# Optimization experiments

Hardware: AMD Instinct MI355X
Metric: run time of the kernel (lower is better)

## Reference

```python
import jax, jax.numpy as jnp
import numpy as np

B, S, D, H, TM = 4, 512, 512, 8, 20
DH = D // H
LAMBDA_REG = 1e-3


def setup_inputs() -> dict:
    key = jax.random.key(0)
    ks = jax.random.split(key, 12)

    def lin(k, o, i):
        return (jax.random.normal(k, (o, i), jnp.float32) / np.float32(np.sqrt(i)))

    return {
        "x": jax.random.normal(ks[0], (B, S, D), jnp.float32),
        "Wq": lin(ks[1], D, D), "Wk": lin(ks[2], D, D), "Wv": lin(ks[3], D, D),
        "Wo": lin(ks[4], D, D), "bo": jnp.zeros((D,), jnp.float32),
        "gw1": lin(ks[5], 64, D), "gb1": jnp.zeros((64,), jnp.float32),
        "gw2": lin(ks[6], 32, 64), "gb2": jnp.zeros((32,), jnp.float32),
        "gw3": lin(ks[7], 1, 32), "gb3": jnp.zeros((1,), jnp.float32),
        "cw1": lin(ks[8], 32, D), "cb1": jnp.zeros((32,), jnp.float32),
        "cw2": lin(ks[9], 1, 32), "cb2": jnp.zeros((1,), jnp.float32),
        "alpha": jnp.float32(np.exp(-1.0 / 5.0)),   # tau_syn = 5
        "beta": jnp.float32(np.exp(-1.0 / 20.0)),   # tau_mem = 20
    }


def reference(x, Wq, Wk, Wv, Wo, bo, gw1, gb1, gw2, gb2, gw3, gb3,
              cw1, cb1, cw2, cb2, alpha, beta):
    scale = jnp.float32(DH ** -0.5)

    # adaptive window sizes T_i in [1, TM]
    g = jax.nn.sigmoid(jax.nn.relu(jax.nn.relu(x @ gw1.T + gb1) @ gw2.T + gb2) @ gw3.T + gb3)
    c = jax.nn.sigmoid(jax.nn.relu(x @ cw1.T + cb1) @ cw2.T + cb2)
    combined = (0.7 * g + 0.3 * c)[..., 0]                       # [B,S]
    T_i = jnp.clip(jnp.ceil(combined * TM), 1, TM).astype(jnp.int32)
    mask = (jnp.arange(TM)[None, None, :] < T_i[:, :, None]).astype(x.dtype)  # [B,S,TM]

    def lif_spikes(inp):  # inp [B,S,D] -> spikes [B,S,TM,D] (zeroed past T_i)
        def step(carry, _):
            v, i = carry
            i = alpha * i + inp
            v = beta * v + i
            s = jnp.where(v >= 1.0, 1.0, 0.0).astype(inp.dtype)
            v = v * (1.0 - s)  # v_reset = 0
            return (v, i), s
        z = jnp.zeros_like(inp)
        _, sp = jax.lax.scan(step, (z, z), None, length=TM)      # [TM,B,S,D]
        return jnp.moveaxis(sp, 0, 2) * mask[..., None]

    q_sp = lif_spikes(x @ Wq.T).reshape(B, S, TM, H, DH)
    k_sp = lif_spikes(x @ Wk.T).reshape(B, S, TM, H, DH)
    v_sp = lif_spikes(x @ Wv.T).reshape(B, S, TM, H, DH)

    scores = jnp.einsum('bithd,bjthd->bhij', q_sp, k_sp) * scale
    attn = jax.nn.softmax(scores, axis=-1)                       # dropout is eval-mode identity
    v_mean = v_sp.mean(axis=2).transpose(0, 2, 1, 3)             # [B,H,S,DH]
    out = jnp.einsum('bhij,bhjd->bhid', attn, v_mean)
    out = out.transpose(0, 2, 1, 3).reshape(B, S, D) @ Wo.T + bo
    reg = jnp.float32(LAMBDA_REG) * T_i.astype(x.dtype).mean()
    return out, attn, reg, T_i
```

## Files before the change

kernel.cpp:

```cpp
#include <hip/hip_runtime.h>
#include <cstdint>


typedef __attribute__((ext_vector_type(8))) _Float16 f16x8;
typedef __attribute__((ext_vector_type(4))) float f32x4;

__device__ __forceinline__ float sep_mad(float a, float b, float c) {
    float t = a * b;
    asm volatile("" : "+v"(t));
    return t + c;
}

union HU4 { _Float16 h[4]; ushort4 u; };
union HU8 { _Float16 h[8]; uint4 u; };

__device__ __forceinline__ void split4(float4 v, HU4& hi, HU4& lo) {
    hi.h[0] = (_Float16)v.x; lo.h[0] = (_Float16)(v.x - (float)hi.h[0]);
    hi.h[1] = (_Float16)v.y; lo.h[1] = (_Float16)(v.y - (float)hi.h[1]);
    hi.h[2] = (_Float16)v.z; lo.h[2] = (_Float16)(v.z - (float)hi.h[2]);
    hi.h[3] = (_Float16)v.w; lo.h[3] = (_Float16)(v.w - (float)hi.h[3]);
}

__global__ __launch_bounds__(256) void k_gemm3(
    const float* __restrict__ X,
    const float* __restrict__ Wq, const float* __restrict__ Wk,
    const float* __restrict__ Wv, const float* __restrict__ gw1,
    const float* __restrict__ cw1,
    float* __restrict__ Y)
{
    __shared__ _Float16 AsH[4][64][8];
    __shared__ _Float16 BsH[4][64][8];
    __shared__ _Float16 AsL[4][64][8];
    __shared__ _Float16 BsL[4][64][8];

    const int bn = blockIdx.x * 64, bm = blockIdx.y * 64;
    const int tid = threadIdx.x, w = tid >> 6, l = tid & 63;
    const int mB = (w & 1) * 32, nB = (w >> 1) * 32;
    const int sr = tid >> 2, sk = tid & 3;
    const int fr = l & 15, fk = l >> 4;

    const float* asrc = X + (bm + sr) * 512;
    const int brow = bn + sr;
    const float* bsrc;
    bool bvalid = true;
    if      (brow < 512)  bsrc = Wq  + brow * 512;
    else if (brow < 1024) bsrc = Wk  + (brow - 512) * 512;
    else if (brow < 1536) bsrc = Wv  + (brow - 1024) * 512;
    else if (brow < 1600) bsrc = gw1 + (brow - 1536) * 512;
    else if (brow < 1632) bsrc = cw1 + (brow - 1600) * 512;
    else { bsrc = Wq; bvalid = false; }

    f32x4 acc[2][2] = {};
    const float4 z4{0.f, 0.f, 0.f, 0.f};

    float4 pa0 = *(const float4*)(asrc + sk * 8);
    float4 pa1 = *(const float4*)(asrc + sk * 8 + 4);
    float4 pb0 = bvalid ? *(const float4*)(bsrc + sk * 8)     : z4;
    float4 pb1 = bvalid ? *(const float4*)(bsrc + sk * 8 + 4) : z4;

    for (int k0 = 0; k0 < 512; k0 += 32) {
        __syncthreads();
        {
            HU4 h0, l0, h1, l1;
            split4(pa0, h0, l0); split4(pa1, h1, l1);
            *(ushort4*)&AsH[sk][sr][0] = h0.u; *(ushort4*)&AsH[sk][sr][4] = h1.u;
            *(ushort4*)&AsL[sk][sr][0] = l0.u; *(ushort4*)&AsL[sk][sr][4] = l1.u;
            split4(pb0, h0, l0); split4(pb1, h1, l1);
            *(ushort4*)&BsH[sk][sr][0] = h0.u; *(ushort4*)&BsH[sk][sr][4] = h1.u;
            *(ushort4*)&BsL[sk][sr][0] = l0.u; *(ushort4*)&BsL[sk][sr][4] = l1.u;
        }
        __syncthreads();
        const int kn = (k0 + 32) & 511;
        pa0 = *(const float4*)(asrc + kn + sk * 8);
        pa1 = *(const float4*)(asrc + kn + sk * 8 + 4);
        if (bvalid) {
            pb0 = *(const float4*)(bsrc + kn + sk * 8);
            pb1 = *(const float4*)(bsrc + kn + sk * 8 + 4);
        }

        f16x8 ah[2], al[2];
#pragma unroll
        for (int mt = 0; mt < 2; mt++) {
            ah[mt] = *(const f16x8*)&AsH[fk][mB + mt * 16 + fr][0];
            al[mt] = *(const f16x8*)&AsL[fk][mB + mt * 16 + fr][0];
        }
#pragma unroll
        for (int nt = 0; nt < 2; nt++) {
            f16x8 bh = *(const f16x8*)&BsH[fk][nB + nt * 16 + fr][0];
            f16x8 bl = *(const f16x8*)&BsL[fk][nB + nt * 16 + fr][0];
#pragma unroll
            for (int mt = 0; mt < 2; mt++) {
                acc[mt][nt] = __builtin_amdgcn_mfma_f32_16x16x32_f16(ah[mt], bh, acc[mt][nt], 0, 0, 0);
                acc[mt][nt] = __builtin_amdgcn_mfma_f32_16x16x32_f16(ah[mt], bl, acc[mt][nt], 0, 0, 0);
                acc[mt][nt] = __builtin_amdgcn_mfma_f32_16x16x32_f16(al[mt], bh, acc[mt][nt], 0, 0, 0);
            }
        }
    }

#pragma unroll
    for (int mt = 0; mt < 2; mt++) {
#pragma unroll
        for (int nt = 0; nt < 2; nt++) {
            const int j = bn + nB + nt * 16 + fr;
#pragma unroll
            for (int rr = 0; rr < 4; rr++) {
                const int i = bm + mB + mt * 16 + fk * 4 + rr;
                Y[i * 1664 + j] = acc[mt][nt][rr];
            }
        }
    }
}

__global__ __launch_bounds__(256) void k_lif(
    const float* __restrict__ qkvh1,
    const float* __restrict__ gb1, const float* __restrict__ cb1,
    const float* __restrict__ gw2, const float* __restrict__ gb2,
    const float* __restrict__ gw3, const float* __restrict__ gb3,
    const float* __restrict__ cw2, const float* __restrict__ cb2,
    const float* __restrict__ pAlpha, const float* __restrict__ pBeta,
    unsigned long long* __restrict__ qbits,
    unsigned long long* __restrict__ kbits,
    _Float16* __restrict__ vmT,
    int* __restrict__ Ti, float* __restrict__ ti_out)
{
    __shared__ _Float16 cnts[64][18];
    __shared__ float h1s[16][100];
    __shared__ float w2s[32][65];
    __shared__ float h2s[16][36];
    __shared__ int tis[16];
    const int tid = threadIdx.x;
    const int wid = tid >> 6, lane = tid & 63;
    const int bh = blockIdx.y, s0 = blockIdx.x * 16;
    const int b = bh >> 3, h = bh & 7;
    const float alpha = pAlpha[0], beta = pBeta[0];

    for (int i = tid; i < 2048; i += 256) w2s[i >> 6][i & 63] = gw2[i];
    for (int i = tid; i < 1536; i += 256) {
        const int r = i / 96, c = i % 96;
        const float v = qkvh1[(long)(b * 512 + s0 + r) * 1664 + 1536 + c]
                        + (c < 64 ? gb1[c] : cb1[c - 64]);
        h1s[r][c] = fmaxf(v, 0.f);
    }
    __syncthreads();
#pragma unroll
    for (int ii = 0; ii < 2; ii++) {
        const int idx = tid + ii * 256;
        const int tok = idx >> 5, o2 = idx & 31;
        float a = gb2[o2];
        for (int k = 0; k < 64; k++) a = fmaf(w2s[o2][k], h1s[tok][k], a);
        h2s[tok][o2] = fmaxf(a, 0.f);
    }
    __syncthreads();
    if (tid < 16) {
        const int tok = tid;
        float gg = gb3[0], cc = cb2[0];
        for (int k = 0; k < 32; k++) {
            gg = fmaf(gw3[k], h2s[tok][k], gg);
            cc = fmaf(cw2[k], h1s[tok][64 + k], cc);
        }
        float g = 1.f / (1.f + expf(-gg));
        float c = 1.f / (1.f + expf(-cc));
        float p1 = 0.7f * g, p2 = 0.3f * c;
        asm volatile("" : "+v"(p1), "+v"(p2));
        float comb = p1 + p2;
        float tf = ceilf(comb * 20.0f);
        tf = fminf(fmaxf(tf, 1.f), 20.f);
        tis[tok] = (int)tf;
        Ti[b * 512 + s0 + tok] = (int)tf;
        ti_out[b * 512 + s0 + tok] = tf;
    }
    __syncthreads();

    const float* qrow0 = qkvh1 + (long)(b * 512 + s0 + wid) * 1664 + h * 64 + lane;
    float cq = qrow0[0], ck = qrow0[512], cv = qrow0[1024];

    for (int r = 0; r < 4; r++) {
        const int tl = r * 4 + wid;
        const int s = s0 + tl;
        float nq = 0.f, nk = 0.f, nv = 0.f;
        if (r < 3) {
            const float* qr = qkvh1 + (long)(b * 512 + s + 4) * 1664 + h * 64 + lane;
            nq = qr[0]; nk = qr[512]; nv = qr[1024];
        }
        const int T = tis[tl];
        float iq = 0.f, vq = 0.f, ik = 0.f, vk = 0.f, iv = 0.f, vv = 0.f;
        int cnt = 0;
        const int base = (bh * 20) * 512 + s;
#pragma unroll
        for (int t = 0; t < 20; t++) {
            iq = sep_mad(alpha, iq, cq); vq = sep_mad(beta, vq, iq);
            bool sq = vq >= 1.0f; vq = sq ? 0.f : vq;
            ik = sep_mad(alpha, ik, ck); vk = sep_mad(beta, vk, ik);
            bool sk = vk >= 1.0f; vk = sk ? 0.f : vk;
            iv = sep_mad(alpha, iv, cv); vv = sep_mad(beta, vv, iv);
            bool sv = vv >= 1.0f; vv = sv ? 0.f : vv;
            bool act = t < T;
            unsigned long long mq = __ballot(sq && act);
            unsigned long long mk = __ballot(sk && act);
            if (lane == 0) {
                qbits[base + t * 512] = mq;
                kbits[base + t * 512] = mk;
            }
            cnt += (sv && act) ? 1 : 0;
        }
        cnts[lane][tl] = (_Float16)((float)cnt / 20.0f);
        cq = nq; ck = nk; cv = nv;
    }
    __syncthreads();
    const int d = tid >> 2, q = tid & 3;
    HU4 o;
#pragma unroll
    for (int i = 0; i < 4; i++) o.h[i] = cnts[d][q * 4 + i];
    *(ushort4*)(vmT + (bh * 64 + d) * 512 + s0 + q * 4) = o.u;
}

__global__ __launch_bounds__(256) void k_scores(
    const unsigned long long* __restrict__ qbits,
    const unsigned long long* __restrict__ kbits,
    float* __restrict__ attn,
    const int* __restrict__ Ti, float* __restrict__ regp)
{
    const int bh = blockIdx.x >> 5;
    const int i0 = (blockIdx.x & 31) * 16;
    const int base = bh * 20 * 512;
    __shared__ unsigned long long qs[20][16];
    __shared__ float sc[16][512];
    const int tid = threadIdx.x;
    for (int idx = tid; idx < 320; idx += 256) {
        int t = idx >> 4, r = idx & 15;
        qs[t][r] = qbits[base + t * 512 + i0 + r];
    }
    int Tmax = 0;
    const int tb = (bh >> 3) * 512 + i0;
#pragma unroll
    for (int r = 0; r < 16; r++) Tmax = max(Tmax, Ti[tb + r]);
    __syncthreads();

    {
        const unsigned long long* kbp = kbits + base + 2 * tid;
        int acc0[16] = {}, acc1[16] = {};
        for (int tc = 0; tc < 4; tc++) {
            if (tc * 5 >= Tmax) break;
            unsigned long long kv0[5], kv1[5];
#pragma unroll
            for (int t = 0; t < 5; t++) {
                ulonglong2 kk = *(const ulonglong2*)(kbp + (tc * 5 + t) * 512);
                kv0[t] = kk.x; kv1[t] = kk.y;
            }
#pragma unroll
            for (int r = 0; r < 16; r++) {
#pragma unroll
                for (int t = 0; t < 5; t++) {
                    unsigned long long qv = qs[tc * 5 + t][r];
                    acc0[r] += __popcll(qv & kv0[t]);
                    acc1[r] += __popcll(qv & kv1[t]);
                }
            }
        }
#pragma unroll
        for (int r = 0; r < 16; r++) {
            sc[r][2 * tid]     = (float)acc0[r] * 0.125f;
            sc[r][2 * tid + 1] = (float)acc1[r] * 0.125f;
        }
    }
    __syncthreads();

    const int wid = tid >> 6, lane = tid & 63;
#pragma unroll
    for (int rr = 0; rr < 4; rr++) {
        const int r = wid * 4 + rr;
        float vals[8];
        float m = -1e30f;
#pragma unroll
        for (int k = 0; k < 8; k++) { vals[k] = sc[r][lane + 64 * k]; m = fmaxf(m, vals[k]); }
#pragma unroll
        for (int off = 32; off; off >>= 1) m = fmaxf(m, __shfl_xor(m, off));
        float sum = 0.f;
#pragma unroll
        for (int k = 0; k < 8; k++) { vals[k] = expf(vals[k] - m); sum += vals[k]; }
#pragma unroll
        for (int off = 32; off; off >>= 1) sum += __shfl_xor(sum, off);
        float* arow = attn + ((long)bh * 512 + (i0 + r)) * 512;
#pragma unroll
        for (int k = 0; k < 8; k++) arow[lane + 64 * k] = vals[k] / sum;
    }

    if (blockIdx.x == 0 && tid < 64) {
        int s = 0;
        for (int k = tid; k < 2048; k += 64) s += Ti[k];
#pragma unroll
        for (int off = 32; off; off >>= 1) s += __shfl_xor(s, off);
        if (tid == 0) regp[0] = 1e-3f * ((float)s / 2048.0f);
    }
}

__global__ __launch_bounds__(256) void k_av(
    const float* __restrict__ attn,
    const _Float16* __restrict__ vmT,
    _Float16* __restrict__ hout)
{
    __shared__ _Float16 Aa[4][64][8];
    __shared__ _Float16 Bb[4][64][8];
    const int i0 = blockIdx.x * 64;
    const int bh = blockIdx.y;
    const int b = bh >> 3, h = bh & 7;
    const int tid = threadIdx.x, w = tid >> 6, l = tid & 63;
    const int mB = (w & 1) * 32, nB = (w >> 1) * 32;
    const int sr = tid >> 2, sk = tid & 3;
    const int fr = l & 15, fk = l >> 4;
    const float* abase = attn + ((long)bh * 512 + i0) * 512;
    const _Float16* bbase = vmT + bh * 64 * 512;

    f32x4 acc[2][2] = {};

    float4 pa0 = *(const float4*)(abase + sr * 512 + sk * 8);
    float4 pa1 = *(const float4*)(abase + sr * 512 + sk * 8 + 4);
    uint4 pb = *(const uint4*)(bbase + sr * 512 + sk * 8);

    for (int k0 = 0; k0 < 512; k0 += 32) {
        __syncthreads();
        {
            HU8 z;
            z.h[0] = (_Float16)pa0.x; z.h[1] = (_Float16)pa0.y;
            z.h[2] = (_Float16)pa0.z; z.h[3] = (_Float16)pa0.w;
            z.h[4] = (_Float16)pa1.x; z.h[5] = (_Float16)pa1.y;
            z.h[6] = (_Float16)pa1.z; z.h[7] = (_Float16)pa1.w;
            *(uint4*)&Aa[sk][sr][0] = z.u;
            *(uint4*)&Bb[sk][sr][0] = pb;
        }
        __syncthreads();
        const int kn = (k0 + 32) & 511;
        pa0 = *(const float4*)(abase + sr * 512 + kn + sk * 8);
        pa1 = *(const float4*)(abase + sr * 512 + kn + sk * 8 + 4);
        pb = *(const uint4*)(bbase + sr * 512 + kn + sk * 8);

        f16x8 ah[2];
#pragma unroll
        for (int mt = 0; mt < 2; mt++)
            ah[mt] = *(const f16x8*)&Aa[fk][mB + mt * 16 + fr][0];
#pragma unroll
        for (int nt = 0; nt < 2; nt++) {
            f16x8 bv = *(const f16x8*)&Bb[fk][nB + nt * 16 + fr][0];
#pragma unroll
            for (int mt = 0; mt < 2; mt++)
                acc[mt][nt] = __builtin_amdgcn_mfma_f32_16x16x32_f16(ah[mt], bv, acc[mt][nt], 0, 0, 0);
        }
    }

#pragma unroll
    for (int mt = 0; mt < 2; mt++) {
#pragma unroll
        for (int nt = 0; nt < 2; nt++) {
            const int d = nB + nt * 16 + fr;
#pragma unroll
            for (int rr = 0; rr < 4; rr++) {
                const int i = i0 + mB + mt * 16 + fk * 4 + rr;
                hout[(b * 512 + i) * 512 + h * 64 + d] = (_Float16)acc[mt][nt][rr];
            }
        }
    }
}

__global__ __launch_bounds__(256) void k_gemmWo(
    const _Float16* __restrict__ A, const float* __restrict__ Wo,
    const float* __restrict__ bias, float* __restrict__ Y)
{
    __shared__ _Float16 As[4][64][8];
    __shared__ _Float16 Bs[4][64][8];

    const int bn = blockIdx.x * 64, bm = blockIdx.y * 64;
    const int tid = threadIdx.x, w = tid >> 6, l = tid & 63;
    const int mB = (w & 1) * 32, nB = (w >> 1) * 32;
    const int sr = tid >> 2, sk = tid & 3;
    const int fr = l & 15, fk = l >> 4;

    f32x4 acc[2][2] = {};

    const float* bsrc = Wo + (bn + sr) * 512;
    uint4 pA = *(const uint4*)(A + (bm + sr) * 512 + sk * 8);
    float4 pb0 = *(const float4*)(bsrc + sk * 8);
    float4 pb1 = *(const float4*)(bsrc + sk * 8 + 4);

    for (int k0 = 0; k0 < 512; k0 += 32) {
        __syncthreads();
        {
            HU8 z;
            z.h[0] = (_Float16)pb0.x; z.h[1] = (_Float16)pb0.y;
            z.h[2] = (_Float16)pb0.z; z.h[3] = (_Float16)pb0.w;
            z.h[4] = (_Float16)pb1.x; z.h[5] = (_Float16)pb1.y;
            z.h[6] = (_Float16)pb1.z; z.h[7] = (_Float16)pb1.w;
            *(uint4*)&As[sk][sr][0] = pA;
            *(uint4*)&Bs[sk][sr][0] = z.u;
        }
        __syncthreads();
        const int kn = (k0 + 32) & 511;
        pA = *(const uint4*)(A + (bm + sr) * 512 + kn + sk * 8);
        pb0 = *(const float4*)(bsrc + kn + sk * 8);
        pb1 = *(const float4*)(bsrc + kn + sk * 8 + 4);

        f16x8 ah[2];
#pragma unroll
        for (int mt = 0; mt < 2; mt++)
            ah[mt] = *(const f16x8*)&As[fk][mB + mt * 16 + fr][0];
#pragma unroll
        for (int nt = 0; nt < 2; nt++) {
            f16x8 bh = *(const f16x8*)&Bs[fk][nB + nt * 16 + fr][0];
#pragma unroll
            for (int mt = 0; mt < 2; mt++)
                acc[mt][nt] = __builtin_amdgcn_mfma_f32_16x16x32_f16(ah[mt], bh, acc[mt][nt], 0, 0, 0);
        }
    }

#pragma unroll
    for (int mt = 0; mt < 2; mt++) {
#pragma unroll
        for (int nt = 0; nt < 2; nt++) {
            const int j = bn + nB + nt * 16 + fr;
            const float badd = bias[j];
#pragma unroll
            for (int rr = 0; rr < 4; rr++) {
                const int i = bm + mB + mt * 16 + fk * 4 + rr;
                Y[i * 512 + j] = acc[mt][nt][rr] + badd;
            }
        }
    }
}

extern "C" void kernel_launch(void* const* d_in, const int* in_sizes, int n_in,
                              void* d_out, int out_size, void* d_ws, size_t ws_size,
                              hipStream_t stream)
{
    const float* x    = (const float*)d_in[0];
    const float* Wq   = (const float*)d_in[1];
    const float* Wk   = (const float*)d_in[2];
    const float* Wv   = (const float*)d_in[3];
    const float* Wo   = (const float*)d_in[4];
    const float* bo   = (const float*)d_in[5];
    const float* gw1  = (const float*)d_in[6];
    const float* gb1  = (const float*)d_in[7];
    const float* gw2  = (const float*)d_in[8];
    const float* gb2  = (const float*)d_in[9];
    const float* gw3  = (const float*)d_in[10];
    const float* gb3  = (const float*)d_in[11];
    const float* cw1  = (const float*)d_in[12];
    const float* cb1  = (const float*)d_in[13];
    const float* cw2  = (const float*)d_in[14];
    const float* cb2  = (const float*)d_in[15];
    const float* alpha = (const float*)d_in[16];
    const float* beta  = (const float*)d_in[17];

    float* out   = (float*)d_out;
    float* attn  = out + 1048576;
    float* regp  = out + 1048576 + 8388608;
    float* tiout = regp + 1;

    char* ws = (char*)d_ws;
    float*    qkvh1  = (float*)ws;
    unsigned long long* qb = (unsigned long long*)(ws + 13631488);
    unsigned long long* kb = (unsigned long long*)(ws + 16252928);
    _Float16* vmT    = (_Float16*)(ws + 18874368);
    _Float16* hout_h = (_Float16*)(ws + 20971520);
    int*      Ti     = (int*)(ws + 23068672);

    k_gemm3<<<dim3(26, 32), 256, 0, stream>>>(x, Wq, Wk, Wv, gw1, cw1, qkvh1);
    k_lif<<<dim3(32, 32), 256, 0, stream>>>(qkvh1, gb1, cb1, gw2, gb2, gw3, gb3,
                                            cw2, cb2, alpha, beta, qb, kb, vmT, Ti, tiout);
    k_scores<<<1024, 256, 0, stream>>>(qb, kb, attn, Ti, regp);
    k_av<<<dim3(8, 32), 256, 0, stream>>>(attn, vmT, hout_h);
    k_gemmWo<<<dim3(8, 32), 256, 0, stream>>>(hout_h, Wo, bo, out);
}
```

Baseline: 109.2 us.

## Fuse attention-times-V into scores kernel and drop split-fp16 for QKV GEMM

The softmax kernel now keeps the normalized attention row block in fp16 shared memory and immediately multiplies it by the spike-mean V with MFMA. This removes the separate k_av launch and its re-read of the full fp32 attention matrix from global memory. Separately, the QKV projection blocks now use a single fp16 MFMA instead of the hi/lo three-product split, which keeps the split only for the gate and complexity columns. That cuts MFMA and shared-memory work, but Q/K/V pre-activations lose precision, which could flip spike thresholds.

```diff
diff --git a/kernel.cpp b/kernel.cpp
--- a/kernel.cpp
+++ b/kernel.cpp
@@ -13,12 +13,18 @@
 
 union HU4 { _Float16 h[4]; ushort4 u; };
 union HU8 { _Float16 h[8]; uint4 u; };
+union HU2 { _Float16 h[2]; unsigned u; };
 
 __device__ __forceinline__ void split4(float4 v, HU4& hi, HU4& lo) {
     hi.h[0] = (_Float16)v.x; lo.h[0] = (_Float16)(v.x - (float)hi.h[0]);
     hi.h[1] = (_Float16)v.y; lo.h[1] = (_Float16)(v.y - (float)hi.h[1]);
     hi.h[2] = (_Float16)v.z; lo.h[2] = (_Float16)(v.z - (float)hi.h[2]);
     hi.h[3] = (_Float16)v.w; lo.h[3] = (_Float16)(v.w - (float)hi.h[3]);
+}
+
+__device__ __forceinline__ void cast4(float4 v, HU4& hi) {
+    hi.h[0] = (_Float16)v.x; hi.h[1] = (_Float16)v.y;
+    hi.h[2] = (_Float16)v.z; hi.h[3] = (_Float16)v.w;
 }
 
 __global__ __launch_bounds__(256) void k_gemm3(
@@ -38,6 +44,7 @@
     const int mB = (w & 1) * 32, nB = (w >> 1) * 32;
     const int sr = tid >> 2, sk = tid & 3;
     const int fr = l & 15, fk = l >> 4;
+    const bool gate = (bn >= 1536);
 
     const float* asrc = X + (bm + sr) * 512;
     const int brow = bn + sr;
@@ -60,7 +67,7 @@
 
     for (int k0 = 0; k0 < 512; k0 += 32) {
         __syncthreads();
-        {
+        if (gate) {
             HU4 h0, l0, h1, l1;
             split4(pa0, h0, l0); split4(pa1, h1, l1);
             *(ushort4*)&AsH[sk][sr][0] = h0.u; *(ushort4*)&AsH[sk][sr][4] = h1.u;
@@ -68,6 +75,12 @@
             split4(pb0, h0, l0); split4(pb1, h1, l1);
             *(ushort4*)&BsH[sk][sr][0] = h0.u; *(ushort4*)&BsH[sk][sr][4] = h1.u;
             *(ushort4*)&BsL[sk][sr][0] = l0.u; *(ushort4*)&BsL[sk][sr][4] = l1.u;
+        } else {
+            HU4 h0, h1;
+            cast4(pa0, h0); cast4(pa1, h1);
+            *(ushort4*)&AsH[sk][sr][0] = h0.u; *(ushort4*)&AsH[sk][sr][4] = h1.u;
+            cast4(pb0, h0); cast4(pb1, h1);
+            *(ushort4*)&BsH[sk][sr][0] = h0.u; *(ushort4*)&BsH[sk][sr][4] = h1.u;
         }
         __syncthreads();
         const int kn = (k0 + 32) & 511;
@@ -78,21 +91,33 @@
             pb1 = *(const float4*)(bsrc + kn + sk * 8 + 4);
         }
 
-        f16x8 ah[2], al[2];
-#pragma unroll
-        for (int mt = 0; mt < 2; mt++) {
+        f16x8 ah[2];
+#pragma unroll
+        for (int mt = 0; mt < 2; mt++)
             ah[mt] = *(const f16x8*)&AsH[fk][mB + mt * 16 + fr][0];
-            al[mt] = *(const f16x8*)&AsL[fk][mB + mt * 16 + fr][0];
-        }
-#pragma unroll
-        for (int nt = 0; nt < 2; nt++) {
-            f16x8 bh = *(const f16x8*)&BsH[fk][nB + nt * 16 + fr][0];
-            f16x8 bl = *(const f16x8*)&BsL[fk][nB + nt * 16 + fr][0];
-#pragma unroll
-            for (int mt = 0; mt < 2; mt++) {
-                acc[mt][nt] = __builtin_amdgcn_mfma_f32_16x16x32_f16(ah[mt], bh, acc[mt][nt], 0, 0, 0);
-                acc[mt][nt] = __builtin_amdgcn_mfma_f32_16x16x32_f16(ah[mt], bl, acc[mt][nt], 0, 0, 0);
-                acc[mt][nt] = __builtin_amdgcn_mfma_f32_16x16x32_f16(al[mt], bh, acc[mt][nt], 0, 0, 0);
+        if (gate) {
+            f16x8 al[2];
+#pragma unroll
+            for (int mt = 0; mt < 2; mt++)
+                al[mt] = *(const f16x8*)&AsL[fk][mB + mt * 16 + fr][0];
+#pragma unroll
+            for (int nt = 0; nt < 2; nt++) {
+                f16x8 bh = *(const f16x8*)&BsH[fk][nB + nt * 16 + fr][0];
+                f16x8 bl = *(const f16x8*)&BsL[fk][nB + nt * 16 + fr][0];
+#pragma unroll
+                for (int mt = 0; mt < 2; mt++) {
+                    acc[mt][nt] = __builtin_amdgcn_mfma_f32_16x16x32_f16(ah[mt], bh, acc[mt][nt], 0, 0, 0);
+                    acc[mt][nt] = __builtin_amdgcn_mfma_f32_16x16x32_f16(ah[mt], bl, acc[mt][nt], 0, 0, 0);
+                    acc[mt][nt] = __builtin_amdgcn_mfma_f32_16x16x32_f16(al[mt], bh, acc[mt][nt], 0, 0, 0);
+                }
+            }
+        } else {
+#pragma unroll
+            for (int nt = 0; nt < 2; nt++) {
+                f16x8 bh = *(const f16x8*)&BsH[fk][nB + nt * 16 + fr][0];
+#pragma unroll
+                for (int mt = 0; mt < 2; mt++)
+                    acc[mt][nt] = __builtin_amdgcn_mfma_f32_16x16x32_f16(ah[mt], bh, acc[mt][nt], 0, 0, 0);
             }
         }
     }
@@ -214,17 +239,19 @@
     *(ushort4*)(vmT + (bh * 64 + d) * 512 + s0 + q * 4) = o.u;
 }
 
-__global__ __launch_bounds__(256) void k_scores(
+__global__ __launch_bounds__(256) void k_scores_av(
     const unsigned long long* __restrict__ qbits,
     const unsigned long long* __restrict__ kbits,
     float* __restrict__ attn,
-    const int* __restrict__ Ti, float* __restrict__ regp)
+    const int* __restrict__ Ti, float* __restrict__ regp,
+    const _Float16* __restrict__ vmT,
+    _Float16* __restrict__ hout)
 {
     const int bh = blockIdx.x >> 5;
     const int i0 = (blockIdx.x & 31) * 16;
     const int base = bh * 20 * 512;
     __shared__ unsigned long long qs[20][16];
-    __shared__ float sc[16][512];
+    __shared__ _Float16 sc16[16][520];
     const int tid = threadIdx.x;
     for (int idx = tid; idx < 320; idx += 256) {
         int t = idx >> 4, r = idx & 15;
@@ -259,8 +286,10 @@
         }
 #pragma unroll
         for (int r = 0; r < 16; r++) {
-            sc[r][2 * tid]     = (float)acc0[r] * 0.125f;
-            sc[r][2 * tid + 1] = (float)acc1[r] * 0.125f;
+            HU2 p;
+            p.h[0] = (_Float16)((float)acc0[r] * 0.125f);
+            p.h[1] = (_Float16)((float)acc1[r] * 0.125f);
+            *(unsigned*)&sc16[r][2 * tid] = p.u;
         }
     }
     __syncthreads();
@@ -272,7 +301,7 @@
         float vals[8];
         float m = -1e30f;
 #pragma unroll
-        for (int k = 0; k < 8; k++) { vals[k] = sc[r][lane + 64 * k]; m = fmaxf(m, vals[k]); }
+        for (int k = 0; k < 8; k++) { vals[k] = (float)sc16[r][lane + 64 * k]; m = fmaxf(m, vals[k]); }
 #pragma unroll
         for (int off = 32; off; off >>= 1) m = fmaxf(m, __shfl_xor(m, off));
         float sum = 0.f;
@@ -282,7 +311,11 @@
         for (int off = 32; off; off >>= 1) sum += __shfl_xor(sum, off);
         float* arow = attn + ((long)bh * 512 + (i0 + r)) * 512;
 #pragma unroll
-        for (int k = 0; k < 8; k++) arow[lane + 64 * k] = vals[k] / sum;
+        for (int k = 0; k < 8; k++) {
+            const float o = vals[k] / sum;
+            arow[lane + 64 * k] = o;
+            sc16[r][lane + 64 * k] = (_Float16)o;
+        }
     }
 
     if (blockIdx.x == 0 && tid < 64) {
@@ -292,72 +325,23 @@
         for (int off = 32; off; off >>= 1) s += __shfl_xor(s, off);
         if (tid == 0) regp[0] = 1e-3f * ((float)s / 2048.0f);
     }
-}
-
-__global__ __launch_bounds__(256) void k_av(
-    const float* __restrict__ attn,
-    const _Float16* __restrict__ vmT,
-    _Float16* __restrict__ hout)
-{
-    __shared__ _Float16 Aa[4][64][8];
-    __shared__ _Float16 Bb[4][64][8];
-    const int i0 = blockIdx.x * 64;
-    const int bh = blockIdx.y;
+    __syncthreads();
+
+    const int fr = lane & 15, fk = lane >> 4;
     const int b = bh >> 3, h = bh & 7;
-    const int tid = threadIdx.x, w = tid >> 6, l = tid & 63;
-    const int mB = (w & 1) * 32, nB = (w >> 1) * 32;
-    const int sr = tid >> 2, sk = tid & 3;
-    const int fr = l & 15, fk = l >> 4;
-    const float* abase = attn + ((long)bh * 512 + i0) * 512;
-    const _Float16* bbase = vmT + bh * 64 * 512;
-
-    f32x4 acc[2][2] = {};
-
-    float4 pa0 = *(const float4*)(abase + sr * 512 + sk * 8);
-    float4 pa1 = *(const float4*)(abase + sr * 512 + sk * 8 + 4);
-    uint4 pb = *(const uint4*)(bbase + sr * 512 + sk * 8);
-
+    f32x4 acc = {};
+    const _Float16* bsrc = vmT + (bh * 64 + wid * 16 + fr) * 512;
+#pragma unroll
     for (int k0 = 0; k0 < 512; k0 += 32) {
-        __syncthreads();
-        {
-            HU8 z;
-            z.h[0] = (_Float16)pa0.x; z.h[1] = (_Float16)pa0.y;
-            z.h[2] = (_Float16)pa0.z; z.h[3] = (_Float16)pa0.w;
-            z.h[4] = (_Float16)pa1.x; z.h[5] = (_Float16)pa1.y;
-            z.h[6] = (_Float16)pa1.z; z.h[7] = (_Float16)pa1.w;
-            *(uint4*)&Aa[sk][sr][0] = z.u;
-            *(uint4*)&Bb[sk][sr][0] = pb;
-        }
-        __syncthreads();
-        const int kn = (k0 + 32) & 511;
-        pa0 = *(const float4*)(abase + sr * 512 + kn + sk * 8);
-        pa1 = *(const float4*)(abase + sr * 512 + kn + sk * 8 + 4);
-        pb = *(const uint4*)(bbase + sr * 512 + kn + sk * 8);
-
-        f16x8 ah[2];
-#pragma unroll
-        for (int mt = 0; mt < 2; mt++)
-            ah[mt] = *(const f16x8*)&Aa[fk][mB + mt * 16 + fr][0];
-#pragma unroll
-        for (int nt = 0; nt < 2; nt++) {
-            f16x8 bv = *(const f16x8*)&Bb[fk][nB + nt * 16 + fr][0];
-#pragma unroll
-            for (int mt = 0; mt < 2; mt++)
-                acc[mt][nt] = __builtin_amdgcn_mfma_f32_16x16x32_f16(ah[mt], bv, acc[mt][nt], 0, 0, 0);
-        }
-    }
-
-#pragma unroll
-    for (int mt = 0; mt < 2; mt++) {
-#pragma unroll
-        for (int nt = 0; nt < 2; nt++) {
-            const int d = nB + nt * 16 + fr;
-#pragma unroll
-            for (int rr = 0; rr < 4; rr++) {
-                const int i = i0 + mB + mt * 16 + fk * 4 + rr;
-                hout[(b * 512 + i) * 512 + h * 64 + d] = (_Float16)acc[mt][nt][rr];
-            }
-        }
+        f16x8 av = *(const f16x8*)&sc16[fr][k0 + fk * 8];
+        f16x8 bv = *(const f16x8*)(bsrc + k0 + fk * 8);
+        acc = __builtin_amdgcn_mfma_f32_16x16x32_f16(av, bv, acc, 0, 0, 0);
+    }
+    const int d = wid * 16 + fr;
+#pragma unroll
+    for (int rr = 0; rr < 4; rr++) {
+        const int i = i0 + fk * 4 + rr;
+        hout[(b * 512 + i) * 512 + h * 64 + d] = (_Float16)acc[rr];
     }
 }
 
@@ -384,13 +368,10 @@
     for (int k0 = 0; k0 < 512; k0 += 32) {
         __syncthreads();
         {
-            HU8 z;
-            z.h[0] = (_Float16)pb0.x; z.h[1] = (_Float16)pb0.y;
-            z.h[2] = (_Float16)pb0.z; z.h[3] = (_Float16)pb0.w;
-            z.h[4] = (_Float16)pb1.x; z.h[5] = (_Float16)pb1.y;
-            z.h[6] = (_Float16)pb1.z; z.h[7] = (_Float16)pb1.w;
+            HU4 h0, h1;
+            cast4(pb0, h0); cast4(pb1, h1);
             *(uint4*)&As[sk][sr][0] = pA;
-            *(uint4*)&Bs[sk][sr][0] = z.u;
+            *(ushort4*)&Bs[sk][sr][0] = h0.u; *(ushort4*)&Bs[sk][sr][4] = h1.u;
         }
         __syncthreads();
         const int kn = (k0 + 32) & 511;
@@ -465,7 +446,6 @@
     k_gemm3<<<dim3(26, 32), 256, 0, stream>>>(x, Wq, Wk, Wv, gw1, cw1, qkvh1);
     k_lif<<<dim3(32, 32), 256, 0, stream>>>(qkvh1, gb1, cb1, gw2, gb2, gw3, gb3,
                                             cw2, cb2, alpha, beta, qb, kb, vmT, Ti, tiout);
-    k_scores<<<1024, 256, 0, stream>>>(qb, kb, attn, Ti, regp);
-    k_av<<<dim3(8, 32), 256, 0, stream>>>(attn, vmT, hout_h);
+    k_scores_av<<<1024, 256, 0, stream>>>(qb, kb, attn, Ti, regp, vmT, hout_h);
     k_gemmWo<<<dim3(8, 32), 256, 0, stream>>>(hout_h, Wo, bo, out);
 }
```

Result: faster. 95.40 us (-12.6%).
